# Kernel tuning notes

Hardware: AMD Instinct MI355X
Metric: run time of the kernel (lower is better)

## Reference

```python
import jax, jax.numpy as jnp
import numpy as np

NEG_INF = -jnp.inf


def setup_inputs() -> dict:
    key = jax.random.key(0)
    k1, k2, k3, k4 = jax.random.split(key, 4)
    B, V = 256, 128000
    logits = jax.random.normal(k1, (B, V), dtype=jnp.float32)
    temperatures = jax.random.uniform(k2, (B,), dtype=jnp.float32, minval=0.5, maxval=1.5)
    top_ks = jax.random.randint(k3, (B,), 0, 1024, dtype=jnp.int32)
    top_ps = jax.random.uniform(k4, (B,), dtype=jnp.float32)
    return {"logits": logits, "temperatures": temperatures, "top_ks": top_ks, "top_ps": top_ps}


def _filtered_logits(logits, temperatures, top_ks, top_ps):
    # Faithful vectorized version of the per-row torch loops.
    B, V = logits.shape
    x = logits.astype(jnp.float32) / temperatures[:, None]

    # Sort each row descending once; reuse for top-k and top-p.
    order = jnp.argsort(-x, axis=-1)                       # [B, V] desc indices
    sorted_x = jnp.take_along_axis(x, order, axis=-1)      # [B, V]
    ranks = jnp.arange(V)[None, :]                         # [1, V]

    # top-k: active only when 0 < k < V (matches torch branch)
    k = top_ks[:, None].astype(jnp.int32)
    topk_active = (k > 0) & (k < V)
    keep_k = jnp.where(topk_active, ranks < k, True)
    sorted_x = jnp.where(keep_k, sorted_x, NEG_INF)

    # top-p on softmax of top-k-filtered logits. Softmax is order-preserving,
    # so sorted probs == softmax of sorted (filtered) logits.
    sorted_probs = jax.nn.softmax(sorted_x, axis=-1)
    cumsum = jnp.cumsum(sorted_probs, axis=-1)
    p = top_ps[:, None]
    cutoff = jnp.sum(cumsum <= p, axis=-1, keepdims=True)  # (cumsum<=p).sum()
    cutoff = jnp.where(cutoff < V, cutoff + 1, cutoff)     # include next token
    topp_active = (p > 0.0) & (p < 1.0)
    keep_p = jnp.where(topp_active, ranks < cutoff, True)
    sorted_x = jnp.where(keep_p, sorted_x, NEG_INF)

    # Unsort back to original token order.
    inv = jnp.argsort(order, axis=-1)
    return jnp.take_along_axis(sorted_x, inv, axis=-1)


def reference(logits, temperatures, top_ks, top_ps):
    x = _filtered_logits(logits, temperatures, top_ks, top_ps)
    probs = jax.nn.softmax(x, axis=-1)
    # Gumbel-max style sampling: argmax(probs / Exp(1)) (torch .exponential_ trick)
    e = jax.random.exponential(jax.random.key(42), probs.shape, dtype=jnp.float32)
    e = jnp.maximum(e, 1e-10)
    return jnp.argmax(probs / e, axis=-1)
```

## Files before the change

kernel.cpp:

```cpp
#include <hip/hip_runtime.h>
#include <stdint.h>

#define VV 128000
#define BLOCK 1024
#define NB 4096
#define CAP 4096
#define THR 2.0f
#define U0  0xC0000000u
#define MSEL 2048
#define NSEG 16
#define CAPSEG 320
#define F4SEG 2000

typedef unsigned long long ull;

__device__ __forceinline__ uint32_t rotl32(uint32_t x, int r){ return (x << r) | (x >> (32 - r)); }

__device__ __forceinline__ float exp_noise(uint32_t f){
  const uint32_t ks0 = 0u, ks1 = 42u, ks2 = 0x1BD11BDAu ^ 0u ^ 42u;
  uint32_t x0 = 0u + ks0;
  uint32_t x1 = f + ks1;
#define R1(r) { x0 += x1; x1 = rotl32(x1, r); x1 ^= x0; }
  R1(13) R1(15) R1(26) R1(6)   x0 += ks1; x1 += ks2 + 1u;
  R1(17) R1(29) R1(16) R1(24)  x0 += ks2; x1 += ks0 + 2u;
  R1(13) R1(15) R1(26) R1(6)   x0 += ks0; x1 += ks1 + 3u;
  R1(17) R1(29) R1(16) R1(24)  x0 += ks1; x1 += ks2 + 4u;
  R1(13) R1(15) R1(26) R1(6)   x0 += ks2; x1 += ks0 + 5u;
#undef R1
  uint32_t bits = x0 ^ x1;
  float u = __uint_as_float((bits >> 9) | 0x3F800000u) - 1.0f;
  float e = -log1pf(-u);
  return fmaxf(e, 1e-10f);
}

__device__ __forceinline__ uint32_t fkey(float x){
  uint32_t u = __float_as_uint(x);
  return u ^ ((u & 0x80000000u) ? 0xFFFFFFFFu : 0x80000000u);
}
__device__ __forceinline__ float keyval(uint32_t k){
  uint32_t bits = (k & 0x80000000u) ? (k ^ 0x80000000u) : ~k;
  return __uint_as_float(bits);
}

__device__ void suffix_scan_u(uint32_t* h, uint32_t* tmp, int tid){
  const int base = tid * 4;
  uint32_t l0=h[base], l1=h[base+1], l2=h[base+2], l3=h[base+3];
  uint32_t s3=l3, s2=l2+s3, s1=l1+s2, s0=l0+s1;
  tmp[tid] = s0; __syncthreads();
  for (int d=1; d<BLOCK; d<<=1){
    uint32_t add = (tid+d<BLOCK) ? tmp[tid+d] : 0u;
    __syncthreads();
    tmp[tid] += add;
    __syncthreads();
  }
  uint32_t E = (tid+1<BLOCK) ? tmp[tid+1] : 0u;
  h[base]=s0+E; h[base+1]=s1+E; h[base+2]=s2+E; h[base+3]=s3+E;
  __syncthreads();
}
__device__ void suffix_scan_f(float* h, float* tmp, int tid){
  const int base = tid * 4;
  float l0=h[base], l1=h[base+1], l2=h[base+2], l3=h[base+3];
  float s3=l3, s2=l2+s3, s1=l1+s2, s0=l0+s1;
  tmp[tid] = s0; __syncthreads();
  for (int d=1; d<BLOCK; d<<=1){
    float add = (tid+d<BLOCK) ? tmp[tid+d] : 0.f;
    __syncthreads();
    tmp[tid] += add;
    __syncthreads();
  }
  float E = (tid+1<BLOCK) ? tmp[tid+1] : 0.f;
  h[base]=s0+E; h[base+1]=s1+E; h[base+2]=s2+E; h[base+3]=s3+E;
  __syncthreads();
}

__device__ uint32_t select_tth_smallest(uint32_t* a, int n, int t){
  for (int i=0;i<t;i++){
    int mi=i; uint32_t mv=a[i];
    for (int j=i+1;j<n;j++) if (a[j]<mv){ mv=a[j]; mi=j; }
    a[mi]=a[i]; a[i]=mv;
  }
  return a[t-1];
}

__device__ void bitonic_sort(ull* a, int N, int tid){
  for (int len=2; len<=N; len<<=1){
    for (int j=len>>1; j>0; j>>=1){
      for (int i=tid; i<N; i+=BLOCK){
        int l = i ^ j;
        if (l > i){
          ull x = a[i], y = a[l];
          bool asc = ((i & len) == 0);
          if (asc ? (x > y) : (x < y)){ a[i]=y; a[l]=x; }
        }
      }
      __syncthreads();
    }
  }
}

#define ROW4R_BEGIN \
    for (int c0 = tid; c0 < VV/4; c0 += BLOCK*4){ \
      float4 qv[4]; int cb[4]; bool gv[4]; \
      _Pragma("unroll") \
      for (int t=0;t<4;t++){ int cc = c0 + t*BLOCK; gv[t] = (cc < VV/4); cb[t] = cc*4; if (gv[t]) qv[t] = rp[cc]; } \
      _Pragma("unroll") \
      for (int t=0;t<4;t++) if (gv[t]){ \
        float vs[4] = {qv[t].x, qv[t].y, qv[t].z, qv[t].w}; \
        _Pragma("unroll") \
        for (int j=0;j<4;j++){ \
          uint32_t u = fkey(vs[j]); \
          uint32_t idx = (uint32_t)(cb[t]+j); \
          (void)idx;
#define ROW4R_END } } }

#define ROW4_BEGIN \
    for (int c0 = tid; c0 < VV/4; c0 += BLOCK*4){ \
      float4 qv[4]; int cb[4]; bool gv[4]; \
      _Pragma("unroll") \
      for (int t=0;t<4;t++){ int cc = c0 + t*BLOCK; gv[t] = (cc < VV/4); cb[t] = cc*4; if (gv[t]) qv[t] = rp[cc]; } \
      _Pragma("unroll") \
      for (int t=0;t<4;t++) if (gv[t]){ \
        float xs[4] = {qv[t].x, qv[t].y, qv[t].z, qv[t].w}; \
        _Pragma("unroll") \
        for (int j=0;j<4;j++){ \
          float x = xs[j]/T; \
          uint32_t u = fkey(x); \
          uint32_t idx = (uint32_t)(cb[t]+j); \
          (void)idx;
#define ROW4_END } } }

__global__ __launch_bounds__(256) void gather_kernel(
    const float* __restrict__ logits, ull* __restrict__ g_cand,
    uint32_t* __restrict__ g_cnt)
{
  const int bid = blockIdx.x;
  const int row = bid >> 4, seg = bid & 15;
  const int tid = threadIdx.x;
  const float4* rp = reinterpret_cast<const float4*>(logits + (size_t)row * VV);
  __shared__ ull buf[CAPSEG];
  __shared__ int cnt;
  if (tid==0) cnt = 0;
  __syncthreads();
  const int c1 = (seg+1)*F4SEG;
  for (int c = seg*F4SEG + tid; c < c1; c += 256){
    float4 q = rp[c];
    float vs[4] = {q.x, q.y, q.z, q.w};
    #pragma unroll
    for (int j=0;j<4;j++){
      if (vs[j] >= THR){
        int pos = atomicAdd(&cnt, 1);
        uint32_t idx = (uint32_t)(c*4 + j);
        if (pos < CAPSEG) buf[pos] = (((ull)fkey(vs[j]))<<32) | (ull)(~idx);
      }
    }
  }
  __syncthreads();
  const int n = min(cnt, CAPSEG);
  ull* dst = g_cand + (size_t)row*(NSEG*CAPSEG) + seg*CAPSEG;
  for (int i=tid;i<n;i+=256) dst[i] = buf[i];
  if (tid==0) g_cnt[row*NSEG + seg] = (uint32_t)cnt;
}

__global__ __launch_bounds__(BLOCK) void sampler_kernel(
    const float* __restrict__ logits, const float* __restrict__ temps,
    const int* __restrict__ topks, const float* __restrict__ topps,
    int* __restrict__ out, const ull* __restrict__ g_cand,
    const uint32_t* __restrict__ g_cnt, int use_ws)
{
  __shared__ __align__(16) uint8_t SM[102400];
  uint32_t* hist  = (uint32_t*)SM;
  uint32_t* hsuf  = (uint32_t*)(SM + 16*1024);
  ull*      srt2  = (ull*)(SM + 32*1024);
  uint32_t* wtot  = (uint32_t*)(SM + 48*1024);
  ull*      ordx  = (ull*)(SM + 50*1024);
  uint32_t* h4    = (uint32_t*)SM;
  ull*      cand  = (ull*)SM;
  uint32_t* h2    = (uint32_t*)(SM + 32*1024);
  ull*      sort2 = (ull*)(SM + 48*1024);
  float*    S     = (float*)SM;
  float*    wf    = (float*)(SM + 16*1024);
  uint32_t* wu    = (uint32_t*)(SM + 64*1024);
  float*    tmpf  = (float*)(SM + 80*1024);
  uint32_t* tmpu  = (uint32_t*)(SM + 84*1024);
  float*    ck    = (float*)(SM + 88*1024);
  ull*      red   = (ull*)(SM + 92*1024);

  __shared__ int s_idx, s_n, s_n2, s_tk, s_ntk, s_tp, s_ntp;
  __shared__ uint32_t s_uk, s_idxk, s_up, s_idxp;
  __shared__ float s_m, s_Zk, s_Ztot;
  __shared__ ull s_K0;
  __shared__ uint32_t s_cs[NSEG];

  const int b   = blockIdx.x;
  const int tid = threadIdx.x;
  const float T = temps[b];
  const int   k = topks[b];
  const float p = topps[b];
  const float* row = logits + (size_t)b * VV;
  const float4* rp = reinterpret_cast<const float4*>(row);
  const bool topk_act = (k > 0) && (k < VV);
  const bool topp_act = (p > 0.0f) && (p < 1.0f);

  if (topk_act && use_ws && k <= BLOCK){
    if (tid < NSEG) s_cs[tid] = g_cnt[b*NSEG + tid];
    __syncthreads();
    int cs[1]; (void)cs;
    int nf = 0; bool ovf = false;
    #pragma unroll
    for (int s=0;s<NSEG;s++){
      int c = (int)s_cs[s];
      if (c > CAPSEG) ovf = true;
      nf += min(c, CAPSEG);
    }
    if (!ovf && nf >= k){
      const ull* gcd = g_cand + (size_t)b*(NSEG*CAPSEG);
      for (int i=tid;i<NB;i+=BLOCK) hist[i]=0u;
      __syncthreads();
      for (int i=tid;i<NSEG*CAPSEG;i+=BLOCK){
        int s = i / CAPSEG;
        int j = i - s*CAPSEG;
        if (j < (int)min(s_cs[s],(uint32_t)CAPSEG)){
          uint32_t u2 = (uint32_t)(gcd[i]>>32);
          uint32_t bu = (u2 - U0) >> 12; if (bu > 4095u) bu = 4095u;
          atomicAdd(&hist[bu], 1u);
        }
      }
      __syncthreads();
      const int lane = tid & 63, wid = tid >> 6;
      const int bb = tid*4;
      uint32_t l0=hist[bb], l1=hist[bb+1], l2=hist[bb+2], l3=hist[bb+3];
      uint32_t s3=l3, s2=l2+s3, s1=l1+s2, s0=l0+s1;
      uint32_t v = s0;
      #pragma unroll
      for (int d=1; d<64; d<<=1){ uint32_t o=__shfl_down(v,d); if (lane+d<64) v += o; }
      if (lane==0) wtot[wid] = v;
      const uint32_t wexcl = v - s0;
      __syncthreads();
      if (wid==0){
        uint32_t w = (lane<16) ? wtot[lane] : 0u;
        uint32_t own = w;
        #pragma unroll
        for (int d=1; d<16; d<<=1){ uint32_t o=__shfl_down(w,d); if (lane+d<16) w += o; }
        if (lane<16) wtot[lane] = w - own;
      }
      __syncthreads();
      const uint32_t E = wtot[wid] + wexcl;
      hsuf[bb]=s0+E; hsuf[bb+1]=s1+E; hsuf[bb+2]=s2+E; hsuf[bb+3]=s3+E;
      if (tid==0) s_idx = 0;
      __syncthreads();
      #pragma unroll
      for (int j=0;j<4;j++){
        int i = bb+j;
        uint32_t a  = hsuf[i];
        uint32_t nn = (i < NB-1) ? hsuf[i+1] : 0u;
        if (a >= (uint32_t)k && nn < (uint32_t)k) s_idx = i;
      }
      __syncthreads();
      const int gam = s_idx;
      const int m = (int)hsuf[gam];
      if (m <= MSEL){
        for (int i=tid;i<NSEG*CAPSEG;i+=BLOCK){
          int s = i / CAPSEG;
          int j = i - s*CAPSEG;
          if (j < (int)min(s_cs[s],(uint32_t)CAPSEG)){
            ull e = gcd[i];
            uint32_t u2 = (uint32_t)(e>>32);
            uint32_t bu = (u2 - U0) >> 12; if (bu > 4095u) bu = 4095u;
            if ((int)bu >= gam){
              uint32_t sub  = atomicSub(&hist[bu], 1u) - 1u;
              uint32_t base = (bu < NB-1) ? hsuf[bu+1] : 0u;
              srt2[base + sub] = e;
            }
          }
        }
        __syncthreads();
        if (tid < m){
          ull K0 = srt2[tid];
          uint32_t u2 = (uint32_t)(K0>>32);
          uint32_t bu = (u2 - U0) >> 12; if (bu > 4095u) bu = 4095u;
          uint32_t base = (bu < NB-1) ? hsuf[bu+1] : 0u;
          uint32_t nb = hsuf[bu] - base;
          int r = (int)base;
          for (uint32_t q=0;q<nb;q++) r += (srt2[base+q] > K0);
          if (r < k){ ordx[r + (r>>4)] = K0; if (r == 0) s_K0 = K0; }
        }
        if (tid+BLOCK < m){
          ull K1 = srt2[tid+BLOCK];
          uint32_t u2 = (uint32_t)(K1>>32);
          uint32_t bu = (u2 - U0) >> 12; if (bu > 4095u) bu = 4095u;
          uint32_t base = (bu < NB-1) ? hsuf[bu+1] : 0u;
          uint32_t nb = hsuf[bu] - base;
          int r = (int)base;
          for (uint32_t q=0;q<nb;q++) r += (srt2[base+q] > K1);
          if (r < k){ ordx[r + (r>>4)] = K1; if (r == 0) s_K0 = K1; }
        }
        __syncthreads();
        if (tid < 64){
          const int kk = k;
          const float xm = keyval((uint32_t)(s_K0>>32)) / T;
          const int base = tid*16;
          float wv[16]; uint32_t lo[16];
          float tot = 0.f;
          #pragma unroll
          for (int q=0;q<16;q++){
            int r = base+q;
            float w = 0.f; uint32_t l = 0u;
            if (r < kk){
              ull K = ordx[r + (r>>4)];
              w = expf(keyval((uint32_t)(K>>32))/T - xm);
              l = (uint32_t)K;
            }
            wv[q]=w; lo[q]=l; tot += w;
          }
          float run = tot;
          #pragma unroll
          for (int d=1; d<64; d<<=1){ float o=__shfl_up(run,d); if (tid>=d) run += o; }
          const float Zk = __shfl(run, 63);
          float ctot = 0.f; float cks[16];
          #pragma unroll
          for (int q=0;q<16;q++){ ctot += wv[q]/Zk; cks[q] = ctot; }
          float crun = ctot;
          #pragma unroll
          for (int d=1; d<64; d<<=1){ float o=__shfl_up(crun,d); if (tid>=d) crun += o; }
          const float cexl = crun - ctot;
          int cnt = 0;
          #pragma unroll
          for (int q=0;q<16;q++){
            int r = base+q;
            if (r < kk && (cks[q]+cexl) <= p) cnt++;
          }
          #pragma unroll
          for (int d=1; d<64; d<<=1) cnt += __shfl_xor(cnt, d);
          int L;
          if (!topp_act) L = kk;
          else L = (cnt >= kk) ? kk : (cnt + 1);
          ull best = 0ull;
          #pragma unroll
          for (int q=0;q<16;q++){
            int r = base+q;
            if (r < L){
              float qv = wv[q] / exp_noise((uint32_t)b * (uint32_t)VV + (~lo[q]));
              ull pk = (((ull)__float_as_uint(qv)) << 32) | (ull)lo[q];
              if (pk > best) best = pk;
            }
          }
          #pragma unroll
          for (int d=1; d<64; d<<=1){ ull o = __shfl_xor(best, d); if (o > best) best = o; }
          if (tid==0) out[b] = (int)(~(uint32_t)(best & 0xFFFFFFFFull));
        }
        return;
      }
      __syncthreads();
    }
  }

  if (topk_act){
    for (int i=tid;i<4*NB;i+=BLOCK) h4[i]=0u;
    __syncthreads();
    ROW4R_BEGIN
      atomicAdd(&h4[((u>>20)<<2) | (uint32_t)(tid&3)], 1u);
    ROW4R_END
    __syncthreads();
    for (int i=tid;i<NB;i+=BLOCK)
      wu[i] = h4[(i<<2)] + h4[(i<<2)|1] + h4[(i<<2)|2] + h4[(i<<2)|3];
    __syncthreads();
    suffix_scan_u(wu, tmpu, tid);
    if (tid==0) s_idx = 0;
    __syncthreads();
    for (int i=tid;i<NB;i+=BLOCK){
      uint32_t a  = wu[i];
      uint32_t nn = (i+1<NB) ? wu[i+1] : 0u;
      if (a >= (uint32_t)k && nn < (uint32_t)k) s_idx = i;
    }
    __syncthreads();
    const uint32_t beta = (uint32_t)s_idx;
    const int n = (int)wu[beta];
    const uint32_t c_above = (beta+1<NB) ? wu[beta+1] : 0u;
    if (n <= CAP){
      if (tid==0) s_n = 0;
      __syncthreads();
      ROW4R_BEGIN
        if ((u>>20) >= beta){
          int pos = atomicAdd(&s_n, 1);
          cand[pos] = (((ull)(~u))<<32) | idx;
        }
      ROW4R_END
      __syncthreads();
      ull* srt; int m;
      if (n <= 1024){ srt = cand; m = n; }
      else {
        for (int i=tid;i<NB;i+=BLOCK) h2[i]=0u;
        __syncthreads();
        for (int i=tid;i<n;i+=BLOCK){
          uint32_t u2 = ~(uint32_t)(cand[i]>>32);
          if ((u2>>20) == beta) atomicAdd(&h2[(u2>>8)&0xFFFu], 1u);
        }
        __syncthreads();
        suffix_scan_u(h2, tmpu, tid);
        const uint32_t kr = (uint32_t)k - c_above;
        if (tid==0) s_idx = 0;
        __syncthreads();
        for (int i=tid;i<NB;i+=BLOCK){
          uint32_t a  = h2[i];
          uint32_t nn = (i+1<NB) ? h2[i+1] : 0u;
          if (a >= kr && nn < kr) s_idx = i;
        }
        __syncthreads();
        const uint32_t gam = (uint32_t)s_idx;
        const int np = (int)(c_above + h2[gam]);
        if (np <= 1024){
          if (tid==0) s_n2 = 0;
          __syncthreads();
          const uint32_t cut24 = (beta<<12) | gam;
          for (int i=tid;i<n;i+=BLOCK){
            ull e = cand[i];
            uint32_t u2 = ~(uint32_t)(e>>32);
            if ((u2>>8) >= cut24){
              int pos = atomicAdd(&s_n2, 1);
              sort2[pos] = e;
            }
          }
          __syncthreads();
          srt = sort2; m = np;
        } else { srt = cand; m = n; }
      }
      int N = 2; while (N < m) N <<= 1;
      for (int i=tid;i<N;i+=BLOCK) if (i >= m) srt[i] = 0xFFFFFFFFFFFFFFFFull;
      __syncthreads();
      bitonic_sort(srt, N, tid);
      const int kk = k;
      const float xm = keyval(~(uint32_t)(srt[0]>>32)) / T;
      float w = 0.f; uint32_t myidx = 0u;
      if (tid < kk){
        ull e = srt[tid];
        myidx = (uint32_t)e;
        float xv = keyval(~(uint32_t)(e>>32)) / T;
        w = expf(xv - xm);
      }
      ck[tid] = w; __syncthreads();
      for (int d=BLOCK/2; d>0; d>>=1){
        if (tid < d) ck[tid] += ck[tid+d];
        __syncthreads();
      }
      if (tid==0) s_Ztot = ck[0];
      __syncthreads();
      const float Zk = s_Ztot;
      ck[tid] = w / Zk; __syncthreads();
      for (int d=1; d<BLOCK; d<<=1){
        float add = (tid >= d) ? ck[tid-d] : 0.f;
        __syncthreads();
        ck[tid] += add;
        __syncthreads();
      }
      tmpu[tid] = (tid < kk && ck[tid] <= p) ? 1u : 0u;
      __syncthreads();
      for (int d=BLOCK/2; d>0; d>>=1){
        if (tid < d) tmpu[tid] += tmpu[tid+d];
        __syncthreads();
      }
      int L;
      if (!topp_act) L = kk;
      else { int c = (int)tmpu[0]; L = (c >= kk) ? kk : (c + 1); }
      ull best = 0ull;
      if (tid < L){
        float q = w / exp_noise((uint32_t)b * (uint32_t)VV + myidx);
        best = (((ull)__float_as_uint(q)) << 32) | (uint32_t)(~myidx);
      }
      red[tid] = best; __syncthreads();
      for (int d=BLOCK/2; d>0; d>>=1){
        if (tid < d){ ull o = red[tid+d]; if (o > red[tid]) red[tid] = o; }
        __syncthreads();
      }
      if (tid==0) out[b] = (int)(~(uint32_t)(red[0] & 0xFFFFFFFFull));
      return;
    }
    __syncthreads();
  }

  for (int i=tid;i<NB;i+=BLOCK){ S[i]=0.f; wu[i]=0u; }
  __syncthreads();
  float lmax = -3.4e38f;
  ROW4_BEGIN
    lmax = fmaxf(lmax, x);
    atomicAdd(&wu[u>>20], 1u);
    atomicAdd(&S[u>>20], expf(x));
  ROW4_END
  tmpf[tid] = lmax; __syncthreads();
  for (int d=BLOCK/2; d>0; d>>=1){
    if (tid < d) tmpf[tid] = fmaxf(tmpf[tid], tmpf[tid+d]);
    __syncthreads();
  }
  if (tid==0) s_m = tmpf[0];
  __syncthreads();
  suffix_scan_u(wu, tmpu, tid);
  suffix_scan_f(S,  tmpf, tid);

  uint32_t uk = 0u, idxk = 0xFFFFFFFFu;
  int bk1 = -1;
  if (topk_act){
    if (tid==0) s_idx = 0;
    __syncthreads();
    for (int i=tid;i<NB;i+=BLOCK){
      uint32_t a  = wu[i];
      uint32_t nn = (i+1<NB) ? wu[i+1] : 0u;
      if (a >= (uint32_t)k && nn < (uint32_t)k) s_idx = i;
    }
    __syncthreads();
    bk1 = s_idx;
    const uint32_t c_above1 = (bk1+1<NB) ? wu[bk1+1] : 0u;
    const float    M_above1 = (bk1+1<NB) ? S[bk1+1]  : 0.f;
    __syncthreads();
    for (int i=tid;i<NB;i+=BLOCK){ wu[i]=0u; wf[i]=0.f; }
    __syncthreads();
    ROW4_BEGIN
      if ((int)(u>>20) == bk1){
        atomicAdd(&wu[(u>>8)&0xFFFu], 1u);
        atomicAdd(&wf[(u>>8)&0xFFFu], expf(x));
      }
    ROW4_END
    __syncthreads();
    suffix_scan_u(wu, tmpu, tid);
    suffix_scan_f(wf, tmpf, tid);
    if (tid==0) s_idx = 0;
    __syncthreads();
    for (int i=tid;i<NB;i+=BLOCK){
      uint32_t a  = c_above1 + wu[i];
      uint32_t nn = c_above1 + ((i+1<NB) ? wu[i+1] : 0u);
      if (a >= (uint32_t)k && nn < (uint32_t)k) s_idx = i;
    }
    __syncthreads();
    const int bk2 = s_idx;
    const uint32_t c_above2 = c_above1 + ((bk2+1<NB) ? wu[bk2+1] : 0u);
    const float    M_above2 = M_above1 + ((bk2+1<NB) ? wf[bk2+1] : 0.f);
    __syncthreads();
    if (tid < 256){ wu[tid]=0u; wf[tid]=0.f; }
    __syncthreads();
    const uint32_t top24k = (((uint32_t)bk1)<<12) | (uint32_t)bk2;
    ROW4_BEGIN
      if ((u>>8) == top24k){
        atomicAdd(&wu[u & 0xFFu], 1u);
        atomicAdd(&wf[u & 0xFFu], expf(x));
      }
    ROW4_END
    __syncthreads();
    if (tid==0){
      uint32_t r = 0u; float mr = 0.f; int b3 = 0;
      for (int i=255;i>=0;--i){
        if (c_above2 + r + wu[i] >= (uint32_t)k){ b3 = i; break; }
        r += wu[i]; mr += wf[i];
      }
      const uint32_t cgt = c_above2 + r;
      const float mgt = M_above2 + mr;
      const int nt = (int)wu[b3];
      const int tk = k - (int)cgt;
      s_uk  = (((uint32_t)bk1)<<20) | (((uint32_t)bk2)<<8) | (uint32_t)b3;
      s_tk  = tk; s_ntk = nt;
      s_Zk  = mgt + (float)tk * expf(keyval(s_uk));
      s_n   = 0;
    }
    __syncthreads();
    uk = s_uk;
    if (s_tk < s_ntk){
      ROW4_BEGIN
        if (u == uk){
          int pos = atomicAdd(&s_n, 1);
          if (pos < NB) wu[pos] = idx;
        }
      ROW4_END
      __syncthreads();
      if (tid==0){
        int n2 = min(s_n, NB);
        int t  = min(s_tk, n2);
        s_idxk = select_tth_smallest(wu, n2, t);
      }
      __syncthreads();
      idxk = s_idxk;
    }
  }
  const float Zk = topk_act ? s_Zk : S[0];

  uint32_t up = 0u, idxp = 0xFFFFFFFFu;
  const float tgt = p * Zk;
  const bool pall = (!topp_act) || (tgt >= Zk);
  if (!pall){
    if (tid==0) s_idx = -2;
    __syncthreads();
    for (int i=tid;i<NB;i+=BLOCK){
      if (i > bk1){
        float a  = S[i];
        float nn = (i+1<NB) ? S[i+1] : 0.f;
        if (a > tgt && nn <= tgt) s_idx = i;
      }
    }
    __syncthreads();
    int bp1 = (s_idx >= 0) ? s_idx : bk1;
    if (bp1 < 0) bp1 = 0;
    const float Mab = (bp1+1<NB) ? S[bp1+1] : 0.f;
    __syncthreads();
    for (int i=tid;i<NB;i+=BLOCK) wf[i]=0.f;
    __syncthreads();
    ROW4_BEGIN
      if ((int)(u>>20) == bp1){
        bool kk_ok = (!topk_act) || (u > uk) || (u == uk && idx <= idxk);
        if (kk_ok) atomicAdd(&wf[(u>>8)&0xFFFu], expf(x));
      }
    ROW4_END
    __syncthreads();
    suffix_scan_f(wf, tmpf, tid);
    if (tid==0) s_idx = -2;
    __syncthreads();
    for (int i=tid;i<NB;i+=BLOCK){
      float a  = Mab + wf[i];
      float nn = Mab + ((i+1<NB) ? wf[i+1] : 0.f);
      if (a > tgt && nn <= tgt) s_idx = i;
    }
    __syncthreads();
    int bp2;
    if (s_idx >= 0){ bp2 = s_idx; }
    else {
      if (tid==0) s_idx = NB;
      __syncthreads();
      for (int i=tid;i<NB;i+=BLOCK){
        float a  = wf[i];
        float nn = (i+1<NB) ? wf[i+1] : 0.f;
        if (a > nn) atomicMin(&s_idx, i);
      }
      __syncthreads();
      bp2 = (s_idx < NB) ? s_idx : 0;
    }
    const float Mab2 = Mab + ((bp2+1<NB) ? wf[bp2+1] : 0.f);
    __syncthreads();
    if (tid < 256){ wf[tid]=0.f; wu[tid]=0u; }
    __syncthreads();
    const uint32_t top24p = (((uint32_t)bp1)<<12) | (uint32_t)bp2;
    ROW4_BEGIN
      if ((u>>8) == top24p){
        bool kk_ok = (!topk_act) || (u > uk) || (u == uk && idx <= idxk);
        if (kk_ok){
          atomicAdd(&wf[u & 0xFFu], expf(x));
          atomicAdd(&wu[u & 0xFFu], 1u);
        }
      }
    ROW4_END
    __syncthreads();
    if (tid==0){
      float run = 0.f; int b3 = -1; float mgt = 0.f;
      for (int i=255;i>=0;--i){
        float sufn = run; run += wf[i];
        if (Mab2 + run > tgt && Mab2 + sufn <= tgt){ b3 = i; mgt = Mab2 + sufn; break; }
      }
      if (b3 < 0){
        float run2 = 0.f;
        for (int i=255;i>=0;--i){
          if (wu[i] > 0u){ b3 = i; mgt = Mab2 + run2; }
          run2 += wf[i];
        }
        if (b3 < 0){ b3 = 0; mgt = Mab2; }
      }
      const uint32_t upv = (((uint32_t)bp1)<<20) | (((uint32_t)bp2)<<8) | (uint32_t)b3;
      const int ntp = (int)wu[b3];
      const float ev = expf(keyval(upv));
      int t = 0;
      for (int j=1;j<=ntp;j++){
        float before = mgt + (float)(j-1) * ev;
        if (before / Zk <= p) t++; else break;
      }
      if (t < 1) t = 1;
      s_up = upv; s_tp = t; s_ntp = ntp; s_n = 0;
    }
    __syncthreads();
    up = s_up;
    if (s_tp < s_ntp){
      ROW4_BEGIN
        if (u == up){
          bool kk_ok = (!topk_act) || (u > uk) || (u == uk && idx <= idxk);
          if (kk_ok){
            int pos = atomicAdd(&s_n, 1);
            if (pos < NB) wu[pos] = idx;
          }
        }
      ROW4_END
      __syncthreads();
      if (tid==0){
        int n2 = min(s_n, NB);
        int t  = min(s_tp, n2);
        s_idxp = select_tth_smallest(wu, n2, t);
      }
      __syncthreads();
      idxp = s_idxp;
    }
  }

  const float m  = s_m;
  const float Zs = Zk * expf(-m);
  ull best = 0ull;
  ROW4_BEGIN
    bool kk_ok = (!topk_act) || (u > uk) || (u == uk && idx <= idxk);
    bool kp_ok = pall || (u > up) || (u == up && idx <= idxp);
    if (kk_ok && kp_ok){
      float q = (expf(x - m) / Zs) / exp_noise((uint32_t)b * (uint32_t)VV + idx);
      ull pk = (((ull)__float_as_uint(q)) << 32) | (uint32_t)(~idx);
      best = (pk > best) ? pk : best;
    }
  ROW4_END
  red[tid] = best; __syncthreads();
  for (int d=BLOCK/2; d>0; d>>=1){
    if (tid < d){ ull o = red[tid+d]; if (o > red[tid]) red[tid] = o; }
    __syncthreads();
  }
  if (tid==0) out[b] = (int)(~(uint32_t)(red[0] & 0xFFFFFFFFull));
}

extern "C" void kernel_launch(void* const* d_in, const int* in_sizes, int n_in,
                              void* d_out, int out_size, void* d_ws, size_t ws_size,
                              hipStream_t stream) {
  (void)in_sizes; (void)n_in; (void)out_size;
  const float* logits = (const float*)d_in[0];
  const float* temps  = (const float*)d_in[1];
  const int*   ks     = (const int*)d_in[2];
  const float* ps     = (const float*)d_in[3];
  int* out = (int*)d_out;

  const size_t cnt_bytes  = 256 * NSEG * sizeof(uint32_t);
  const size_t cand_bytes = (size_t)256 * NSEG * CAPSEG * sizeof(ull);
  const size_t need = cnt_bytes + cand_bytes;

  uint32_t* g_cnt  = (uint32_t*)d_ws;
  ull*      g_cand = (ull*)((uint8_t*)d_ws + cnt_bytes);
  const int use_ws = (d_ws != nullptr && ws_size >= need) ? 1 : 0;

  if (use_ws)
    gather_kernel<<<256*NSEG, 256, 0, stream>>>(logits, g_cand, g_cnt);
  sampler_kernel<<<256, BLOCK, 0, stream>>>(logits, temps, ks, ps, out,
                                            g_cand, g_cnt, use_ws);
}
```

Before: 211.8 us.

## Fuse candidate gather with last-block top-k selection via global completion counter

The per-segment gather and the fast-path top-k/top-p selection now live in one kernel. The last of a row's 16 segment blocks, found with an atomic done counter and threadfence, runs the selection using histograms and sort buffers held in global workspace. The full-row sweep kernel exits early for rows already finished and only handles fallback rows. This is meant to cut the 1024-thread sampler's fast-path work and its serialization behind the gather. The cost is an extra memset, selection done by 256 threads with global-memory atomics, and a larger workspace requirement.

```diff
diff --git a/kernel.cpp b/kernel.cpp
--- a/kernel.cpp
+++ b/kernel.cpp
@@ -129,50 +129,217 @@
           (void)idx;
 #define ROW4_END } } }
 
-__global__ __launch_bounds__(256) void gather_kernel(
-    const float* __restrict__ logits, ull* __restrict__ g_cand,
-    uint32_t* __restrict__ g_cnt)
+__global__ __launch_bounds__(256) void fused_kernel(
+    const float* __restrict__ logits, const float* __restrict__ temps,
+    const int* __restrict__ topks, const float* __restrict__ topps,
+    int* __restrict__ out,
+    ull* __restrict__ g_cand, uint32_t* __restrict__ g_cnt,
+    uint32_t* __restrict__ g_done, uint32_t* __restrict__ g_ok,
+    uint32_t* __restrict__ g_hist, uint32_t* __restrict__ g_hsuf,
+    ull* __restrict__ g_srt)
 {
   const int bid = blockIdx.x;
   const int row = bid >> 4, seg = bid & 15;
   const int tid = threadIdx.x;
-  const float4* rp = reinterpret_cast<const float4*>(logits + (size_t)row * VV);
-  __shared__ ull buf[CAPSEG];
-  __shared__ int cnt;
-  if (tid==0) cnt = 0;
-  __syncthreads();
-  const int c1 = (seg+1)*F4SEG;
-  for (int c = seg*F4SEG + tid; c < c1; c += 256){
-    float4 q = rp[c];
-    float vs[4] = {q.x, q.y, q.z, q.w};
+
+  __shared__ __align__(16) uint8_t SMu[8704];
+  ull* buf  = (ull*)SMu;
+  ull* ordx = (ull*)SMu;
+  __shared__ int s_cnt, s_last, s_gam, s_m;
+  __shared__ ull s_K0;
+  __shared__ uint32_t s_cs[NSEG];
+  __shared__ uint32_t wtot4[4];
+
+  if (tid==0) s_cnt = 0;
+  __syncthreads();
+  {
+    const float4* rp = reinterpret_cast<const float4*>(logits + (size_t)row * VV);
+    const int c1 = (seg+1)*F4SEG;
+    for (int c = seg*F4SEG + tid; c < c1; c += 256){
+      float4 q = rp[c];
+      float vs[4] = {q.x, q.y, q.z, q.w};
+      #pragma unroll
+      for (int j=0;j<4;j++){
+        if (vs[j] >= THR){
+          int pos = atomicAdd(&s_cnt, 1);
+          uint32_t idx = (uint32_t)(c*4 + j);
+          if (pos < CAPSEG) buf[pos] = (((ull)fkey(vs[j]))<<32) | (ull)(~idx);
+        }
+      }
+    }
+  }
+  __syncthreads();
+  {
+    const int n = min(s_cnt, CAPSEG);
+    ull* dst = g_cand + (size_t)row*(NSEG*CAPSEG) + seg*CAPSEG;
+    for (int i=tid;i<n;i+=256) dst[i] = buf[i];
+    if (tid==0) g_cnt[row*NSEG + seg] = (uint32_t)s_cnt;
+  }
+  __syncthreads();
+  if (tid==0){
+    __threadfence();
+    uint32_t old = atomicAdd(&g_done[row], 1u);
+    s_last = (old == (uint32_t)(NSEG-1)) ? 1 : 0;
+  }
+  __syncthreads();
+  if (!s_last) return;
+  __threadfence();
+
+  const float T = temps[row];
+  const int   k = topks[row];
+  const float p = topps[row];
+  const bool topk_act = (k > 0) && (k < VV);
+  const bool topp_act = (p > 0.0f) && (p < 1.0f);
+
+  if (tid < NSEG) s_cs[tid] = g_cnt[row*NSEG + tid];
+  __syncthreads();
+  bool ovf = false;
+  #pragma unroll
+  for (int s=0;s<NSEG;s++) if (s_cs[s] > (uint32_t)CAPSEG) ovf = true;
+  if (!topk_act || k > 1024 || ovf){
+    if (tid==0) g_ok[row] = 0u;
+    return;
+  }
+
+  uint32_t* hist = g_hist + (size_t)row*NB;
+  uint32_t* hsuf = g_hsuf + (size_t)row*NB;
+  ull*      srt  = g_srt  + (size_t)row*MSEL;
+  const ull* gcd = g_cand + (size_t)row*(NSEG*CAPSEG);
+
+  for (int i=tid;i<NB;i+=256) hist[i] = 0u;
+  __syncthreads();
+  for (int i=tid;i<NSEG*CAPSEG;i+=256){
+    int s = i / CAPSEG;
+    int j = i - s*CAPSEG;
+    if (j < (int)s_cs[s]){
+      uint32_t u2 = (uint32_t)(gcd[i]>>32);
+      uint32_t bu = (u2 - U0) >> 12; if (bu > 4095u) bu = 4095u;
+      atomicAdd(&hist[bu], 1u);
+    }
+  }
+  __syncthreads();
+
+  const int lane = tid & 63, wid = tid >> 6;
+  const int b16 = tid*16;
+  uint32_t h[16], suf[16];
+  uint32_t run = 0u;
+  #pragma unroll
+  for (int j=15;j>=0;--j){ h[j] = hist[b16+j]; run += h[j]; suf[j] = run; }
+  uint32_t v = run;
+  #pragma unroll
+  for (int d=1; d<64; d<<=1){ uint32_t o = __shfl_down(v,d); if (lane+d<64) v += o; }
+  if (lane==0) wtot4[wid] = v;
+  const uint32_t wexcl = v - run;
+  if (tid==0) s_gam = -1;
+  __syncthreads();
+  uint32_t E = wexcl;
+  #pragma unroll
+  for (int w=0; w<4; ++w) if (w > wid) E += wtot4[w];
+  #pragma unroll
+  for (int j=0;j<16;j++){
+    uint32_t a  = suf[j] + E;
+    hsuf[b16+j] = a;
+    hist[b16+j] = a;
+    uint32_t nn = a - h[j];
+    if (a >= (uint32_t)k && nn < (uint32_t)k){ s_gam = b16+j; s_m = (int)a; }
+  }
+  __syncthreads();
+  const int gam = s_gam;
+  if (gam < 0){ if (tid==0) g_ok[row] = 0u; return; }
+  const int m = s_m;
+  if (m > MSEL){ if (tid==0) g_ok[row] = 0u; return; }
+
+  for (int i=tid;i<NSEG*CAPSEG;i+=256){
+    int s = i / CAPSEG;
+    int j = i - s*CAPSEG;
+    if (j < (int)s_cs[s]){
+      ull e = gcd[i];
+      uint32_t u2 = (uint32_t)(e>>32);
+      uint32_t bu = (u2 - U0) >> 12; if (bu > 4095u) bu = 4095u;
+      if ((int)bu >= gam){
+        uint32_t pos = atomicSub(&hist[bu], 1u) - 1u;
+        srt[pos] = e;
+      }
+    }
+  }
+  __syncthreads();
+
+  for (int i=tid;i<m;i+=256){
+    ull e = srt[i];
+    uint32_t u2 = (uint32_t)(e>>32);
+    uint32_t bu = (u2 - U0) >> 12; if (bu > 4095u) bu = 4095u;
+    uint32_t base = (bu < (uint32_t)(NB-1)) ? hsuf[bu+1] : 0u;
+    uint32_t nb = hsuf[bu] - base;
+    int r = (int)base;
+    for (uint32_t q=0;q<nb;q++) r += (srt[base+q] > e);
+    if (r < k){ ordx[r + (r>>4)] = e; if (r == 0) s_K0 = e; }
+  }
+  __syncthreads();
+
+  if (tid < 64){
+    const int kk = k;
+    const float xm = keyval((uint32_t)(s_K0>>32)) / T;
+    const int base = tid*16;
+    float wv[16]; uint32_t lo[16];
+    float tot = 0.f;
     #pragma unroll
-    for (int j=0;j<4;j++){
-      if (vs[j] >= THR){
-        int pos = atomicAdd(&cnt, 1);
-        uint32_t idx = (uint32_t)(c*4 + j);
-        if (pos < CAPSEG) buf[pos] = (((ull)fkey(vs[j]))<<32) | (ull)(~idx);
-      }
-    }
-  }
-  __syncthreads();
-  const int n = min(cnt, CAPSEG);
-  ull* dst = g_cand + (size_t)row*(NSEG*CAPSEG) + seg*CAPSEG;
-  for (int i=tid;i<n;i+=256) dst[i] = buf[i];
-  if (tid==0) g_cnt[row*NSEG + seg] = (uint32_t)cnt;
-}
-
-__global__ __launch_bounds__(BLOCK) void sampler_kernel(
+    for (int q=0;q<16;q++){
+      int r = base+q;
+      float w = 0.f; uint32_t l = 0u;
+      if (r < kk){
+        ull K = ordx[r + (r>>4)];
+        w = expf(keyval((uint32_t)(K>>32))/T - xm);
+        l = (uint32_t)K;
+      }
+      wv[q]=w; lo[q]=l; tot += w;
+    }
+    float runl = tot;
+    #pragma unroll
+    for (int d=1; d<64; d<<=1){ float o=__shfl_up(runl,d); if (tid>=d) runl += o; }
+    const float Zk = __shfl(runl, 63);
+    float ctot = 0.f; float cks[16];
+    #pragma unroll
+    for (int q=0;q<16;q++){ ctot += wv[q]/Zk; cks[q] = ctot; }
+    float crun = ctot;
+    #pragma unroll
+    for (int d=1; d<64; d<<=1){ float o=__shfl_up(crun,d); if (tid>=d) crun += o; }
+    const float cexl = crun - ctot;
+    int cnt = 0;
+    #pragma unroll
+    for (int q=0;q<16;q++){
+      int r = base+q;
+      if (r < kk && (cks[q]+cexl) <= p) cnt++;
+    }
+    #pragma unroll
+    for (int d=1; d<64; d<<=1) cnt += __shfl_xor(cnt, d);
+    int L;
+    if (!topp_act) L = kk;
+    else L = (cnt >= kk) ? kk : (cnt + 1);
+    ull best = 0ull;
+    #pragma unroll
+    for (int q=0;q<16;q++){
+      int r = base+q;
+      if (r < L){
+        float qv = wv[q] / exp_noise((uint32_t)row * (uint32_t)VV + (~lo[q]));
+        ull pk = (((ull)__float_as_uint(qv)) << 32) | (ull)lo[q];
+        if (pk > best) best = pk;
+      }
+    }
+    #pragma unroll
+    for (int d=1; d<64; d<<=1){ ull o = __shfl_xor(best, d); if (o > best) best = o; }
+    if (tid==0) out[row] = (int)(~(uint32_t)(best & 0xFFFFFFFFull));
+  }
+  if (tid==0) g_ok[row] = 1u;
+}
+
+__global__ __launch_bounds__(BLOCK) void sweep_kernel(
     const float* __restrict__ logits, const float* __restrict__ temps,
     const int* __restrict__ topks, const float* __restrict__ topps,
-    int* __restrict__ out, const ull* __restrict__ g_cand,
-    const uint32_t* __restrict__ g_cnt, int use_ws)
+    int* __restrict__ out, const uint32_t* __restrict__ g_ok, int use_ws)
 {
+  if (use_ws && g_ok[blockIdx.x] != 0u) return;
+
   __shared__ __align__(16) uint8_t SM[102400];
-  uint32_t* hist  = (uint32_t*)SM;
-  uint32_t* hsuf  = (uint32_t*)(SM + 16*1024);
-  ull*      srt2  = (ull*)(SM + 32*1024);
-  uint32_t* wtot  = (uint32_t*)(SM + 48*1024);
-  ull*      ordx  = (ull*)(SM + 50*1024);
   uint32_t* h4    = (uint32_t*)SM;
   ull*      cand  = (ull*)SM;
   uint32_t* h2    = (uint32_t*)(SM + 32*1024);
@@ -188,8 +355,6 @@
   __shared__ int s_idx, s_n, s_n2, s_tk, s_ntk, s_tp, s_ntp;
   __shared__ uint32_t s_uk, s_idxk, s_up, s_idxp;
   __shared__ float s_m, s_Zk, s_Ztot;
-  __shared__ ull s_K0;
-  __shared__ uint32_t s_cs[NSEG];
 
   const int b   = blockIdx.x;
   const int tid = threadIdx.x;
@@ -200,159 +365,6 @@
   const float4* rp = reinterpret_cast<const float4*>(row);
   const bool topk_act = (k > 0) && (k < VV);
   const bool topp_act = (p > 0.0f) && (p < 1.0f);
-
-  if (topk_act && use_ws && k <= BLOCK){
-    if (tid < NSEG) s_cs[tid] = g_cnt[b*NSEG + tid];
-    __syncthreads();
-    int cs[1]; (void)cs;
-    int nf = 0; bool ovf = false;
-    #pragma unroll
-    for (int s=0;s<NSEG;s++){
-      int c = (int)s_cs[s];
-      if (c > CAPSEG) ovf = true;
-      nf += min(c, CAPSEG);
-    }
-    if (!ovf && nf >= k){
-      const ull* gcd = g_cand + (size_t)b*(NSEG*CAPSEG);
-      for (int i=tid;i<NB;i+=BLOCK) hist[i]=0u;
-      __syncthreads();
-      for (int i=tid;i<NSEG*CAPSEG;i+=BLOCK){
-        int s = i / CAPSEG;
-        int j = i - s*CAPSEG;
-        if (j < (int)min(s_cs[s],(uint32_t)CAPSEG)){
-          uint32_t u2 = (uint32_t)(gcd[i]>>32);
-          uint32_t bu = (u2 - U0) >> 12; if (bu > 4095u) bu = 4095u;
-          atomicAdd(&hist[bu], 1u);
-        }
-      }
-      __syncthreads();
-      const int lane = tid & 63, wid = tid >> 6;
-      const int bb = tid*4;
-      uint32_t l0=hist[bb], l1=hist[bb+1], l2=hist[bb+2], l3=hist[bb+3];
-      uint32_t s3=l3, s2=l2+s3, s1=l1+s2, s0=l0+s1;
-      uint32_t v = s0;
-      #pragma unroll
-      for (int d=1; d<64; d<<=1){ uint32_t o=__shfl_down(v,d); if (lane+d<64) v += o; }
-      if (lane==0) wtot[wid] = v;
-      const uint32_t wexcl = v - s0;
-      __syncthreads();
-      if (wid==0){
-        uint32_t w = (lane<16) ? wtot[lane] : 0u;
-        uint32_t own = w;
-        #pragma unroll
-        for (int d=1; d<16; d<<=1){ uint32_t o=__shfl_down(w,d); if (lane+d<16) w += o; }
-        if (lane<16) wtot[lane] = w - own;
-      }
-      __syncthreads();
-      const uint32_t E = wtot[wid] + wexcl;
-      hsuf[bb]=s0+E; hsuf[bb+1]=s1+E; hsuf[bb+2]=s2+E; hsuf[bb+3]=s3+E;
-      if (tid==0) s_idx = 0;
-      __syncthreads();
-      #pragma unroll
-      for (int j=0;j<4;j++){
-        int i = bb+j;
-        uint32_t a  = hsuf[i];
-        uint32_t nn = (i < NB-1) ? hsuf[i+1] : 0u;
-        if (a >= (uint32_t)k && nn < (uint32_t)k) s_idx = i;
-      }
-      __syncthreads();
-      const int gam = s_idx;
-      const int m = (int)hsuf[gam];
-      if (m <= MSEL){
-        for (int i=tid;i<NSEG*CAPSEG;i+=BLOCK){
-          int s = i / CAPSEG;
-          int j = i - s*CAPSEG;
-          if (j < (int)min(s_cs[s],(uint32_t)CAPSEG)){
-            ull e = gcd[i];
-            uint32_t u2 = (uint32_t)(e>>32);
-            uint32_t bu = (u2 - U0) >> 12; if (bu > 4095u) bu = 4095u;
-            if ((int)bu >= gam){
-              uint32_t sub  = atomicSub(&hist[bu], 1u) - 1u;
-              uint32_t base = (bu < NB-1) ? hsuf[bu+1] : 0u;
-              srt2[base + sub] = e;
-            }
-          }
-        }
-        __syncthreads();
-        if (tid < m){
-          ull K0 = srt2[tid];
-          uint32_t u2 = (uint32_t)(K0>>32);
-          uint32_t bu = (u2 - U0) >> 12; if (bu > 4095u) bu = 4095u;
-          uint32_t base = (bu < NB-1) ? hsuf[bu+1] : 0u;
-          uint32_t nb = hsuf[bu] - base;
-          int r = (int)base;
-          for (uint32_t q=0;q<nb;q++) r += (srt2[base+q] > K0);
-          if (r < k){ ordx[r + (r>>4)] = K0; if (r == 0) s_K0 = K0; }
-        }
-        if (tid+BLOCK < m){
-          ull K1 = srt2[tid+BLOCK];
-          uint32_t u2 = (uint32_t)(K1>>32);
-          uint32_t bu = (u2 - U0) >> 12; if (bu > 4095u) bu = 4095u;
-          uint32_t base = (bu < NB-1) ? hsuf[bu+1] : 0u;
-          uint32_t nb = hsuf[bu] - base;
-          int r = (int)base;
-          for (uint32_t q=0;q<nb;q++) r += (srt2[base+q] > K1);
-          if (r < k){ ordx[r + (r>>4)] = K1; if (r == 0) s_K0 = K1; }
-        }
-        __syncthreads();
-        if (tid < 64){
-          const int kk = k;
-          const float xm = keyval((uint32_t)(s_K0>>32)) / T;
-          const int base = tid*16;
-          float wv[16]; uint32_t lo[16];
-          float tot = 0.f;
-          #pragma unroll
-          for (int q=0;q<16;q++){
-            int r = base+q;
-            float w = 0.f; uint32_t l = 0u;
-            if (r < kk){
-              ull K = ordx[r + (r>>4)];
-              w = expf(keyval((uint32_t)(K>>32))/T - xm);
-              l = (uint32_t)K;
-            }
-            wv[q]=w; lo[q]=l; tot += w;
-          }
-          float run = tot;
-          #pragma unroll
-          for (int d=1; d<64; d<<=1){ float o=__shfl_up(run,d); if (tid>=d) run += o; }
-          const float Zk = __shfl(run, 63);
-          float ctot = 0.f; float cks[16];
-          #pragma unroll
-          for (int q=0;q<16;q++){ ctot += wv[q]/Zk; cks[q] = ctot; }
-          float crun = ctot;
-          #pragma unroll
-          for (int d=1; d<64; d<<=1){ float o=__shfl_up(crun,d); if (tid>=d) crun += o; }
-          const float cexl = crun - ctot;
-          int cnt = 0;
-          #pragma unroll
-          for (int q=0;q<16;q++){
-            int r = base+q;
-            if (r < kk && (cks[q]+cexl) <= p) cnt++;
-          }
-          #pragma unroll
-          for (int d=1; d<64; d<<=1) cnt += __shfl_xor(cnt, d);
-          int L;
-          if (!topp_act) L = kk;
-          else L = (cnt >= kk) ? kk : (cnt + 1);
-          ull best = 0ull;
-          #pragma unroll
-          for (int q=0;q<16;q++){
-            int r = base+q;
-            if (r < L){
-              float qv = wv[q] / exp_noise((uint32_t)b * (uint32_t)VV + (~lo[q]));
-              ull pk = (((ull)__float_as_uint(qv)) << 32) | (ull)lo[q];
-              if (pk > best) best = pk;
-            }
-          }
-          #pragma unroll
-          for (int d=1; d<64; d<<=1){ ull o = __shfl_xor(best, d); if (o > best) best = o; }
-          if (tid==0) out[b] = (int)(~(uint32_t)(best & 0xFFFFFFFFull));
-        }
-        return;
-      }
-      __syncthreads();
-    }
-  }
 
   if (topk_act){
     for (int i=tid;i<4*NB;i+=BLOCK) h4[i]=0u;
@@ -721,16 +733,31 @@
   const float* ps     = (const float*)d_in[3];
   int* out = (int*)d_out;
 
-  const size_t cnt_bytes  = 256 * NSEG * sizeof(uint32_t);
-  const size_t cand_bytes = (size_t)256 * NSEG * CAPSEG * sizeof(ull);
-  const size_t need = cnt_bytes + cand_bytes;
-
-  uint32_t* g_cnt  = (uint32_t*)d_ws;
-  ull*      g_cand = (ull*)((uint8_t*)d_ws + cnt_bytes);
-  const int use_ws = (d_ws != nullptr && ws_size >= need) ? 1 : 0;
-
-  if (use_ws)
-    gather_kernel<<<256*NSEG, 256, 0, stream>>>(logits, g_cand, g_cnt);
-  sampler_kernel<<<256, BLOCK, 0, stream>>>(logits, temps, ks, ps, out,
-                                            g_cand, g_cnt, use_ws);
-}
+  const size_t OFF_CNT  = 0;
+  const size_t OFF_DONE = OFF_CNT  + 16*1024;
+  const size_t OFF_OK   = OFF_DONE + 1024;
+  const size_t OFF_HIST = OFF_OK   + 1024;
+  const size_t OFF_HSUF = OFF_HIST + (size_t)256*NB*4;
+  const size_t OFF_CAND = OFF_HSUF + (size_t)256*NB*4;
+  const size_t OFF_SRT  = OFF_CAND + (size_t)256*NSEG*CAPSEG*8;
+  const size_t WS_TOTAL = OFF_SRT  + (size_t)256*MSEL*8;
+
+  uint8_t* ws = (uint8_t*)d_ws;
+  const int use_ws = (d_ws != nullptr && ws_size >= WS_TOTAL) ? 1 : 0;
+
+  uint32_t* g_cnt  = (uint32_t*)(ws + OFF_CNT);
+  uint32_t* g_done = (uint32_t*)(ws + OFF_DONE);
+  uint32_t* g_ok   = (uint32_t*)(ws + OFF_OK);
+  uint32_t* g_hist = (uint32_t*)(ws + OFF_HIST);
+  uint32_t* g_hsuf = (uint32_t*)(ws + OFF_HSUF);
+  ull*      g_cand = (ull*)     (ws + OFF_CAND);
+  ull*      g_srt  = (ull*)     (ws + OFF_SRT);
+
+  if (use_ws){
+    hipMemsetAsync(g_done, 0, 256*sizeof(uint32_t), stream);
+    fused_kernel<<<256*NSEG, 256, 0, stream>>>(logits, temps, ks, ps, out,
+                                               g_cand, g_cnt, g_done, g_ok,
+                                               g_hist, g_hsuf, g_srt);
+  }
+  sweep_kernel<<<256, BLOCK, 0, stream>>>(logits, temps, ks, ps, out, g_ok, use_ws);
+}
```

Measured after the change: 778.3 us. +267.5%, slower.

## Replace 4096-bin histogram sort with 256-bin threshold and brute-force rank selection

Applied to the files above, without the earlier changes.

The top-k selection over workspace candidates now builds a 256-bin histogram instead of a 4096-bin one, scanned by a single wavefront instead of a block-wide two-level scan. Candidates are held in registers across the histogram and compaction passes, so global memory is read once instead of twice. Candidates at or above the threshold bin are compacted with an atomic counter, and each one's rank is computed by comparing against all m selected keys rather than within its own bucket. This removes several barriers and scan passes, but the rank loop now costs O(m) per thread instead of O(bucket size).

```diff
diff --git a/kernel.cpp b/kernel.cpp
--- a/kernel.cpp
+++ b/kernel.cpp
@@ -168,11 +168,9 @@
     const uint32_t* __restrict__ g_cnt, int use_ws)
 {
   __shared__ __align__(16) uint8_t SM[102400];
-  uint32_t* hist  = (uint32_t*)SM;
-  uint32_t* hsuf  = (uint32_t*)(SM + 16*1024);
-  ull*      srt2  = (ull*)(SM + 32*1024);
-  uint32_t* wtot  = (uint32_t*)(SM + 48*1024);
-  ull*      ordx  = (ull*)(SM + 50*1024);
+  ull*      sel   = (ull*)SM;
+  ull*      ordx  = (ull*)(SM + 16*1024);
+  uint32_t* hco   = (uint32_t*)(SM + 25*1024);
   uint32_t* h4    = (uint32_t*)SM;
   ull*      cand  = (ull*)SM;
   uint32_t* h2    = (uint32_t*)(SM + 32*1024);
@@ -185,7 +183,7 @@
   float*    ck    = (float*)(SM + 88*1024);
   ull*      red   = (ull*)(SM + 92*1024);
 
-  __shared__ int s_idx, s_n, s_n2, s_tk, s_ntk, s_tp, s_ntp;
+  __shared__ int s_idx, s_n, s_n2, s_tk, s_ntk, s_tp, s_ntp, s_b8, s_m2, s_ns;
   __shared__ uint32_t s_uk, s_idxk, s_up, s_idxp;
   __shared__ float s_m, s_Zk, s_Ztot;
   __shared__ ull s_K0;
@@ -203,97 +201,70 @@
 
   if (topk_act && use_ws && k <= BLOCK){
     if (tid < NSEG) s_cs[tid] = g_cnt[b*NSEG + tid];
-    __syncthreads();
-    int cs[1]; (void)cs;
-    int nf = 0; bool ovf = false;
+    if (tid < 256) hco[tid] = 0u;
+    if (tid==0){ s_b8 = -1; s_ns = 0; }
+    __syncthreads();
+    bool ovf = false;
     #pragma unroll
-    for (int s=0;s<NSEG;s++){
-      int c = (int)s_cs[s];
-      if (c > CAPSEG) ovf = true;
-      nf += min(c, CAPSEG);
-    }
-    if (!ovf && nf >= k){
+    for (int s=0;s<NSEG;s++) if (s_cs[s] > (uint32_t)CAPSEG) ovf = true;
+    if (!ovf){
       const ull* gcd = g_cand + (size_t)b*(NSEG*CAPSEG);
-      for (int i=tid;i<NB;i+=BLOCK) hist[i]=0u;
-      __syncthreads();
-      for (int i=tid;i<NSEG*CAPSEG;i+=BLOCK){
+      ull ev[5]; uint32_t bq[5]; bool val[5];
+      #pragma unroll
+      for (int q=0;q<5;q++){
+        int i = tid + q*BLOCK;
         int s = i / CAPSEG;
         int j = i - s*CAPSEG;
-        if (j < (int)min(s_cs[s],(uint32_t)CAPSEG)){
-          uint32_t u2 = (uint32_t)(gcd[i]>>32);
-          uint32_t bu = (u2 - U0) >> 12; if (bu > 4095u) bu = 4095u;
-          atomicAdd(&hist[bu], 1u);
-        }
-      }
-      __syncthreads();
-      const int lane = tid & 63, wid = tid >> 6;
-      const int bb = tid*4;
-      uint32_t l0=hist[bb], l1=hist[bb+1], l2=hist[bb+2], l3=hist[bb+3];
-      uint32_t s3=l3, s2=l2+s3, s1=l1+s2, s0=l0+s1;
-      uint32_t v = s0;
-      #pragma unroll
-      for (int d=1; d<64; d<<=1){ uint32_t o=__shfl_down(v,d); if (lane+d<64) v += o; }
-      if (lane==0) wtot[wid] = v;
-      const uint32_t wexcl = v - s0;
-      __syncthreads();
-      if (wid==0){
-        uint32_t w = (lane<16) ? wtot[lane] : 0u;
-        uint32_t own = w;
+        bool v = (i < NSEG*CAPSEG) && (j < (int)s_cs[s]);
+        val[q] = v; ev[q] = 0ull; bq[q] = 0u;
+        if (v){
+          ull e = gcd[i];
+          ev[q] = e;
+          uint32_t d = (uint32_t)(e>>32) - U0;
+          uint32_t bu = d >> 16; if (bu > 255u) bu = 255u;
+          bq[q] = bu;
+          atomicAdd(&hco[bu], 1u);
+        }
+      }
+      __syncthreads();
+      if (tid < 64){
+        const int b4 = tid*4;
+        uint32_t h0=hco[b4], h1=hco[b4+1], h2v=hco[b4+2], h3=hco[b4+3];
+        uint32_t u3=h3, u2s=h2v+u3, u1=h1+u2s, u0=h0+u1;
+        uint32_t v = u0;
         #pragma unroll
-        for (int d=1; d<16; d<<=1){ uint32_t o=__shfl_down(w,d); if (lane+d<16) w += o; }
-        if (lane<16) wtot[lane] = w - own;
-      }
-      __syncthreads();
-      const uint32_t E = wtot[wid] + wexcl;
-      hsuf[bb]=s0+E; hsuf[bb+1]=s1+E; hsuf[bb+2]=s2+E; hsuf[bb+3]=s3+E;
-      if (tid==0) s_idx = 0;
-      __syncthreads();
-      #pragma unroll
-      for (int j=0;j<4;j++){
-        int i = bb+j;
-        uint32_t a  = hsuf[i];
-        uint32_t nn = (i < NB-1) ? hsuf[i+1] : 0u;
-        if (a >= (uint32_t)k && nn < (uint32_t)k) s_idx = i;
-      }
-      __syncthreads();
-      const int gam = s_idx;
-      const int m = (int)hsuf[gam];
-      if (m <= MSEL){
-        for (int i=tid;i<NSEG*CAPSEG;i+=BLOCK){
-          int s = i / CAPSEG;
-          int j = i - s*CAPSEG;
-          if (j < (int)min(s_cs[s],(uint32_t)CAPSEG)){
-            ull e = gcd[i];
-            uint32_t u2 = (uint32_t)(e>>32);
-            uint32_t bu = (u2 - U0) >> 12; if (bu > 4095u) bu = 4095u;
-            if ((int)bu >= gam){
-              uint32_t sub  = atomicSub(&hist[bu], 1u) - 1u;
-              uint32_t base = (bu < NB-1) ? hsuf[bu+1] : 0u;
-              srt2[base + sub] = e;
-            }
+        for (int d=1; d<64; d<<=1){ uint32_t o=__shfl_down(v,d); if (tid+d<64) v += o; }
+        const uint32_t E = v - u0;
+        uint32_t a0=u0+E, a1=u1+E, a2=u2s+E, a3=u3+E;
+        const uint32_t kk = (uint32_t)k;
+        if (a0 >= kk && a1 < kk){ s_b8 = b4;   s_m2 = (int)a0; }
+        if (a1 >= kk && a2 < kk){ s_b8 = b4+1; s_m2 = (int)a1; }
+        if (a2 >= kk && a3 < kk){ s_b8 = b4+2; s_m2 = (int)a2; }
+        if (a3 >= kk && E  < kk){ s_b8 = b4+3; s_m2 = (int)a3; }
+      }
+      __syncthreads();
+      const int B8 = s_b8;
+      const int m  = s_m2;
+      if (B8 >= 0 && m <= MSEL){
+        #pragma unroll
+        for (int q=0;q<5;q++){
+          if (val[q] && bq[q] >= (uint32_t)B8){
+            int pos = atomicAdd(&s_ns, 1);
+            sel[pos] = ev[q];
           }
         }
         __syncthreads();
-        if (tid < m){
-          ull K0 = srt2[tid];
-          uint32_t u2 = (uint32_t)(K0>>32);
-          uint32_t bu = (u2 - U0) >> 12; if (bu > 4095u) bu = 4095u;
-          uint32_t base = (bu < NB-1) ? hsuf[bu+1] : 0u;
-          uint32_t nb = hsuf[bu] - base;
-          int r = (int)base;
-          for (uint32_t q=0;q<nb;q++) r += (srt2[base+q] > K0);
-          if (r < k){ ordx[r + (r>>4)] = K0; if (r == 0) s_K0 = K0; }
-        }
-        if (tid+BLOCK < m){
-          ull K1 = srt2[tid+BLOCK];
-          uint32_t u2 = (uint32_t)(K1>>32);
-          uint32_t bu = (u2 - U0) >> 12; if (bu > 4095u) bu = 4095u;
-          uint32_t base = (bu < NB-1) ? hsuf[bu+1] : 0u;
-          uint32_t nb = hsuf[bu] - base;
-          int r = (int)base;
-          for (uint32_t q=0;q<nb;q++) r += (srt2[base+q] > K1);
-          if (r < k){ ordx[r + (r>>4)] = K1; if (r == 0) s_K0 = K1; }
-        }
+        ull K0 = (tid < m)       ? sel[tid]       : 0ull;
+        ull K1 = (tid+BLOCK < m) ? sel[tid+BLOCK] : 0ull;
+        int r0 = 0, r1 = 0;
+        #pragma unroll 4
+        for (int j=0;j<m;j++){
+          ull Kj = sel[j];
+          r0 += (Kj > K0);
+          r1 += (Kj > K1);
+        }
+        if (tid < m && r0 < k){ ordx[r0 + (r0>>4)] = K0; if (r0 == 0) s_K0 = K0; }
+        if (tid+BLOCK < m && r1 < k){ ordx[r1 + (r1>>4)] = K1; if (r1 == 0) s_K0 = K1; }
         __syncthreads();
         if (tid < 64){
           const int kk = k;
@@ -312,10 +283,10 @@
             }
             wv[q]=w; lo[q]=l; tot += w;
           }
-          float run = tot;
+          float runl = tot;
           #pragma unroll
-          for (int d=1; d<64; d<<=1){ float o=__shfl_up(run,d); if (tid>=d) run += o; }
-          const float Zk = __shfl(run, 63);
+          for (int d=1; d<64; d<<=1){ float o=__shfl_up(runl,d); if (tid>=d) runl += o; }
+          const float Zk = __shfl(runl, 63);
           float ctot = 0.f; float cks[16];
           #pragma unroll
           for (int q=0;q<16;q++){ ctot += wv[q]/Zk; cks[q] = ctot; }
```

Result: slower. 248.0 us (+17.1%).
